# Kernel optimization log

Measured on AMD Instinct MI355X. Metric: run time of the kernel, lower is better.

Reference implementation:

```python
import jax, jax.numpy as jnp
import numpy as np

N = 65536
E = 1048576
IN_DIM = 128
POS_DIM = 128  # num_nodes (ROI one-hot dim)
HID = 128


def _mk_params(key):
    # layer 0: local in = IN_DIM + POS_DIM; layer 1: local in = HID + POS_DIM
    dims = [(IN_DIM + POS_DIM, HID), (HID + POS_DIM, HID)]
    params = {}
    for l, (din, _) in enumerate(dims):
        ks = jax.random.split(jax.random.fold_in(key, l), 4)
        params[f"l{l}_lw1"] = jax.random.normal(ks[0], (din, HID), jnp.float32) * (1.0 / np.sqrt(din))
        params[f"l{l}_lb1"] = jnp.zeros((HID,), jnp.float32)
        params[f"l{l}_lw2"] = jax.random.normal(ks[1], (HID, HID), jnp.float32) * (1.0 / np.sqrt(HID))
        params[f"l{l}_lb2"] = jnp.zeros((HID,), jnp.float32)
        params[f"l{l}_gw1"] = jax.random.normal(ks[2], (HID, HID), jnp.float32) * (1.0 / np.sqrt(HID))
        params[f"l{l}_gb1"] = jnp.zeros((HID,), jnp.float32)
        params[f"l{l}_gw2"] = jax.random.normal(ks[3], (HID, HID), jnp.float32) * (1.0 / np.sqrt(HID))
        params[f"l{l}_gb2"] = jnp.zeros((HID,), jnp.float32)
    return params


def setup_inputs() -> dict:
    key = jax.random.key(0)
    k1, k2, k3, k4 = jax.random.split(key, 4)
    inp = {
        "x": jax.random.normal(k1, (N, IN_DIM), jnp.float32),
        "pos": jax.random.normal(k2, (N, POS_DIM), jnp.float32),
        "edge_index": jax.random.randint(k3, (2, E), 0, N, jnp.int64),
    }
    inp.update(_mk_params(k4))
    return inp


def _pointnet_conv(x, pos, src, dst, lw1, lb1, lw2, lb2, gw1, gb1, gw2, gb2):
    # message: concat(x_j, pos_j - pos_i) per edge -> local_nn (Lin-ReLU-Lin)
    msg = jnp.concatenate([x[src], pos[src] - pos[dst]], axis=1)  # [E', in+pos]
    h = jax.nn.relu(msg @ lw1 + lb1) @ lw2 + lb2                  # [E', HID]
    agg = jax.ops.segment_max(h, dst, num_segments=N)             # max aggr (PointNetConv default)
    return jax.nn.relu(agg @ gw1 + gb1) @ gw2 + gb2               # global_nn


def reference(x, pos, edge_index,
              l0_lw1, l0_lb1, l0_lw2, l0_lb2, l0_gw1, l0_gb1, l0_gw2, l0_gb2,
              l1_lw1, l1_lb1, l1_lw2, l1_lb2, l1_gw1, l1_gb1, l1_gw2, l1_gb2):
    # add_self_loops=True (PointNetConv default); ensures every node has an incoming edge
    loops = jnp.arange(N, dtype=edge_index.dtype)
    src = jnp.concatenate([edge_index[0], loops])
    dst = jnp.concatenate([edge_index[1], loops])
    h = _pointnet_conv(x, pos, src, dst, l0_lw1, l0_lb1, l0_lw2, l0_lb2,
                       l0_gw1, l0_gb1, l0_gw2, l0_gb2)
    h = _pointnet_conv(h, pos, src, dst, l1_lw1, l1_lb1, l1_lw2, l1_lb2,
                       l1_gw1, l1_gb1, l1_gw2, l1_gb2)
    return h
```

## Files before the change

### kernel.cpp

```cpp
#include <hip/hip_runtime.h>
#include <hip/hip_bf16.h>
#include <stdint.h>

#define NN 65536
#define NE 1048576
#define E2 (NE + NN)
#define HID 128
#define LP 136
#define RMAX 13
#define TP 129
#define TABW 1680
#define ENC_NEG 0x007FFFFFu

typedef _Float16 h8v __attribute__((ext_vector_type(8)));
typedef __fp16 fp16x2 __attribute__((ext_vector_type(2)));
typedef __attribute__((ext_vector_type(4))) float f32x4;

__device__ __forceinline__ uint32_t pkh(float a, float b){
    union { fp16x2 h; uint32_t u; } v;
    v.h = __builtin_amdgcn_cvt_pkrtz(a, b);
    return v.u;
}
__device__ __forceinline__ uint32_t encf(float x){
    union { float f; uint32_t u; } v; v.f = x;
    return v.u ^ (uint32_t)(((int32_t)v.u >> 31) | 0x80000000);
}
__device__ __forceinline__ float decf(uint32_t u){
    union { uint32_t u; float f; } v;
    v.u = u ^ (uint32_t)(~((int32_t)u >> 31) | 0x80000000);
    return v.f;
}

__device__ __forceinline__ void gl_lds16(const _Float16* g, _Float16* l){
    __builtin_amdgcn_global_load_lds(
        (const __attribute__((address_space(1))) uint32_t*)g,
        (__attribute__((address_space(3))) uint32_t*)l, 16, 0, 0);
}

__device__ __forceinline__ void stage_copy(const _Float16* g, _Float16* l){
    const uint4* gs = (const uint4*)g; uint4* ls = (uint4*)l;
    #pragma unroll
    for (int j = 0; j < 8; j++) ls[j] = gs[j];
}
__device__ __forceinline__ void stage_cvt(const float* g, _Float16* l){
    const float4* gs = (const float4*)g; uint4* ls = (uint4*)l;
    #pragma unroll
    for (int j = 0; j < 8; j++){
        float4 f0 = gs[2*j], f1 = gs[2*j+1];
        uint4 o; o.x = pkh(f0.x, f0.y); o.y = pkh(f0.z, f0.w);
        o.z = pkh(f1.x, f1.y); o.w = pkh(f1.z, f1.w);
        ls[j] = o;
    }
}

__device__ __forceinline__ void gemm_tile(const _Float16* Ts, const _Float16* Ws,
                                          f32x4 (&acc)[2][8], int wv, int lq, int quad){
    #pragma unroll
    for (int k0 = 0; k0 < 128; k0 += 32){
        h8v af[2], bfr[8];
        #pragma unroll
        for (int rt = 0; rt < 2; rt++)
            af[rt] = *(const h8v*)(Ts + (wv*32 + rt*16 + lq)*LP + k0 + quad*8);
        #pragma unroll
        for (int ct = 0; ct < 8; ct++)
            bfr[ct] = *(const h8v*)(Ws + (ct*16 + lq)*LP + k0 + quad*8);
        #pragma unroll
        for (int rt = 0; rt < 2; rt++)
            #pragma unroll
            for (int ct = 0; ct < 8; ct++)
                acc[rt][ct] = __builtin_amdgcn_mfma_f32_16x16x32_f16(
                                  af[rt], bfr[ct], acc[rt][ct], 0, 0, 0);
    }
}

__device__ __forceinline__ void zero_acc(f32x4 (&acc)[2][8]){
    #pragma unroll
    for (int a = 0; a < 2; a++)
        #pragma unroll
        for (int b = 0; b < 8; b++)
            acc[a][b] = (f32x4){0.f, 0.f, 0.f, 0.f};
}

struct WT { const float* s[10]; _Float16* d[10]; };
__global__ void k_prep(WT w, uint32_t* cnt,
                       const float* lb2_0, const float* gw1_0, const float* gb1_0,
                       const float* lb2_1, const float* gw1_1, const float* gb1_1,
                       float* c1p){
    int b = blockIdx.x;
    if (b < 640){
        int m = b >> 6;
        int t = (b & 63) * 256 + threadIdx.x;
        int n = t >> 7, k = t & 127;
        w.d[m][n*128 + k] = (_Float16)w.s[m][k*128 + n];
    } else if (b < 896){
        cnt[(b - 640)*256 + threadIdx.x] = 1u;
    } else {
        int l = b - 896;
        int j = threadIdx.x;
        if (j < 128){
            const float* lb2 = l ? lb2_1 : lb2_0;
            const float* gw1 = l ? gw1_1 : gw1_0;
            float s = (l ? gb1_1 : gb1_0)[j];
            for (int k = 0; k < 128; k++) s += lb2[k] * gw1[k*128 + j];
            c1p[l*128 + j] = s;
        }
    }
}

__launch_bounds__(256, 2)
__global__ void k_histab3(const int* __restrict__ ei, uint32_t* __restrict__ cnt,
                          const float* __restrict__ x, const float* __restrict__ pos,
                          const _Float16* __restrict__ w1aT0, const _Float16* __restrict__ w1bT0,
                          const _Float16* __restrict__ w1bT1, const float* __restrict__ lb1_0,
                          _Float16* __restrict__ Ah, _Float16* __restrict__ Bh0,
                          _Float16* __restrict__ Bh1, uint32_t* __restrict__ agg){
    __shared__ _Float16 Ts[128*LP];
    __shared__ _Float16 Ws[128*LP];
    __shared__ float b1s[128];
    const int tid = threadIdx.x;

    if (blockIdx.x >= 512){
        int e = (blockIdx.x - 512) * 256 + tid;
        atomicAdd(&cnt[ei[NE + e]], 1u);
        return;
    }

    const int node0 = blockIdx.x * 128;
    if (tid < 128) b1s[tid] = lb1_0[tid];

    {
        uint4* ap = (uint4*)(agg + (size_t)node0 * HID);
        uint4 v = make_uint4(ENC_NEG, ENC_NEG, ENC_NEG, ENC_NEG);
        #pragma unroll
        for (int i = 0; i < 16; i++) ap[tid + i*256] = v;
    }

    const int row = tid >> 1, half = tid & 1;
    _Float16* lT = Ts + row*LP + half*64;
    _Float16* lW = Ws + row*LP + half*64;

    stage_cvt(pos + (size_t)(node0 + row)*HID + half*64, lT);
    stage_copy(w1bT0 + row*HID + half*64, lW);
    __syncthreads();

    const int wv = tid >> 6, lane = tid & 63, lq = lane & 15, quad = lane >> 4;
    f32x4 acc0[2][8], acc1[2][8];
    zero_acc(acc0);
    gemm_tile(Ts, Ws, acc0, wv, lq, quad);
    __syncthreads();

    #pragma unroll
    for (int rt = 0; rt < 2; rt++)
        #pragma unroll
        for (int ct = 0; ct < 8; ct++)
            #pragma unroll
            for (int rg = 0; rg < 4; rg++){
                int r = node0 + wv*32 + rt*16 + quad*4 + rg;
                int c = ct*16 + lq;
                Bh0[(size_t)r*HID + c] = (_Float16)acc0[rt][ct][rg];
            }
    stage_copy(w1bT1 + row*HID + half*64, lW);
    __syncthreads();

    zero_acc(acc1);
    gemm_tile(Ts, Ws, acc1, wv, lq, quad);
    __syncthreads();

    #pragma unroll
    for (int rt = 0; rt < 2; rt++)
        #pragma unroll
        for (int ct = 0; ct < 8; ct++)
            #pragma unroll
            for (int rg = 0; rg < 4; rg++){
                int r = node0 + wv*32 + rt*16 + quad*4 + rg;
                int c = ct*16 + lq;
                Bh1[(size_t)r*HID + c] = (_Float16)acc1[rt][ct][rg];
            }
    stage_cvt(x + (size_t)(node0 + row)*HID + half*64, lT);
    stage_copy(w1aT0 + row*HID + half*64, lW);
    __syncthreads();

    gemm_tile(Ts, Ws, acc0, wv, lq, quad);

    #pragma unroll
    for (int rt = 0; rt < 2; rt++)
        #pragma unroll
        for (int ct = 0; ct < 8; ct++)
            #pragma unroll
            for (int rg = 0; rg < 4; rg++){
                int r = node0 + wv*32 + rt*16 + quad*4 + rg;
                int c = ct*16 + lq;
                Ah[(size_t)r*HID + c] = (_Float16)(acc0[rt][ct][rg] + b1s[c]);
            }
}

__global__ void k_scan1(const uint32_t* __restrict__ cnt, uint32_t* __restrict__ bsum){
    __shared__ uint32_t ps[256];
    int t = threadIdx.x;
    ps[t] = cnt[blockIdx.x*256 + t]; __syncthreads();
    for (int off = 128; off > 0; off >>= 1){
        if (t < off) ps[t] += ps[t + off];
        __syncthreads();
    }
    if (t == 0) bsum[blockIdx.x] = ps[0];
}
__global__ void k_scan23(const uint32_t* __restrict__ cnt, const uint32_t* __restrict__ bsum,
                         uint32_t* __restrict__ cur){
    __shared__ uint32_t ps[256];
    __shared__ uint32_t bs[256];
    int t = threadIdx.x, b = blockIdx.x, i = b*256 + t;
    uint32_t bb = bsum[b];
    bs[t] = bsum[t];
    uint32_t v = cnt[i];
    ps[t] = v; __syncthreads();
    for (int off = 1; off < 256; off <<= 1){
        uint32_t u = (t >= off) ? ps[t - off] : 0u;
        uint32_t w = (t >= off) ? bs[t - off] : 0u;
        __syncthreads();
        ps[t] += u; bs[t] += w;
        __syncthreads();
    }
    cur[i] = (bs[b] - bb) + ps[t] - v;
}
__global__ void k_scatter(const int* __restrict__ ei, uint32_t* cur,
                          uint2* __restrict__ sedge){
    int e = blockIdx.x * 256 + threadIdx.x;
    if (e >= E2) return;
    uint32_t s, d;
    if (e < NE){ s = (uint32_t)ei[e]; d = (uint32_t)ei[NE + e]; }
    else { s = d = (uint32_t)(e - NE); }
    uint32_t p = atomicAdd(&cur[d], 1u);
    sedge[p] = make_uint2(s, d);
}

__launch_bounds__(256, 4)
__global__ void k_edge(const uint2* __restrict__ sedge,
                       const _Float16* __restrict__ Ah, const _Float16* __restrict__ Bh,
                       const _Float16* __restrict__ w2T,
                       uint32_t* __restrict__ agg){
    __shared__ _Float16 Ws[128*128];
    __shared__ __align__(16) uint32_t tab[TABW];
    __shared__ int ds_s[128];
    __shared__ unsigned long long masks_s[2];
    __shared__ int run_dst_s[RMAX];
    const int tid = threadIdx.x;
    const int bid = blockIdx.x;
    const int lb  = (bid & 7) * (E2/128/8) + (bid >> 3);
    const int e0 = lb * 128;
    const int wv = tid >> 6, lane = tid & 63, lq = lane & 15, quad = lane >> 4;
    const int r0 = wv*32 + lq, r1 = r0 + 16;

    const uint2 ea = sedge[e0 + r0];
    const uint2 eb = sedge[e0 + r1];
    int d_cur = 0;
    if (tid < 128) d_cur = (int)sedge[e0 + tid].y;

    #pragma unroll
    for (int rnd = 0; rnd < 8; rnd++){
        int g = rnd*256 + wv*64 + lane;
        int r = g >> 4, kc = g & 15;
        gl_lds16(w2T + r*HID + ((kc ^ (r & 15)) << 3),
                 Ws + rnd*2048 + wv*512);
    }

    const _Float16* a0p = Ah + (size_t)ea.x*HID + quad*8;
    const _Float16* a1p = Ah + (size_t)eb.x*HID + quad*8;
    const _Float16* b0p = Bh + (size_t)ea.y*HID + quad*8;
    const _Float16* b1p = Bh + (size_t)eb.y*HID + quad*8;
    h8v A0[4], A1[4], B0[4], B1[4];
    #pragma unroll
    for (int i = 0; i < 4; i++){
        A0[i] = *(const h8v*)(a0p + 32*i);
        A1[i] = *(const h8v*)(a1p + 32*i);
        B0[i] = *(const h8v*)(b0p + 32*i);
        B1[i] = *(const h8v*)(b1p + 32*i);
    }

    bool flag = false;
    if (tid < 128){
        ds_s[tid] = d_cur;
        int d_up  = __shfl_up(d_cur, 1);
        int d_b63 = __shfl((int)eb.y, 15);
        if (tid & 63) flag = (d_cur != d_up);
        else          flag = (tid == 0) ? true : (d_cur != d_b63);
        unsigned long long m = __ballot(flag);
        if ((tid & 63) == 0) masks_s[tid >> 6] = m;
    }
    {
        uint4* t4 = (uint4*)tab;
        const uint4 vneg = make_uint4(ENC_NEG, ENC_NEG, ENC_NEG, ENC_NEG);
        #pragma unroll
        for (int i = 0; i < 2; i++){
            int idx = tid + i*256;
            if (idx < TABW/4) t4[idx] = vneg;
        }
    }
    __syncthreads();

    const unsigned long long m0 = masks_s[0], m1 = masks_s[1];
    const int c0 = __popcll(m0);
    const int nruns = c0 + __popcll(m1);

    if (flag){
        int r;
        if (tid < 64) r = __popcll(m0 & ((2ull << tid) - 1)) - 1;
        else          r = c0 + __popcll(m1 & ((2ull << (tid-64)) - 1)) - 1;
        if (r < RMAX) run_dst_s[r] = d_cur;
    }

    f32x4 acc[2][8];
    zero_acc(acc);

    const h8v zero8 = (h8v)(_Float16)0;
    #pragma unroll
    for (int i = 0; i < 4; i++){
        h8v a0 = __builtin_elementwise_max(A0[i] - B0[i], zero8);
        h8v a1 = __builtin_elementwise_max(A1[i] - B1[i], zero8);
        const int kcb = i*4;
        #pragma unroll
        for (int ct = 0; ct < 8; ct++){
            h8v b = *(const h8v*)(Ws + (ct*16 + lq)*128 + (((kcb + quad) ^ lq) << 3));
            acc[0][ct] = __builtin_amdgcn_mfma_f32_16x16x32_f16(a0, b, acc[0][ct], 0, 0, 0);
            acc[1][ct] = __builtin_amdgcn_mfma_f32_16x16x32_f16(a1, b, acc[1][ct], 0, 0, 0);
        }
    }

    #pragma unroll
    for (int rt = 0; rt < 2; rt++){
        const int rb = wv*32 + rt*16 + quad*4;
        int rid[4];
        #pragma unroll
        for (int i = 0; i < 4; i++){
            int r = rb + i;
            if (r < 64) rid[i] = __popcll(m0 & ((2ull << r) - 1)) - 1;
            else        rid[i] = c0 + __popcll(m1 & ((2ull << (r-64)) - 1)) - 1;
        }
        const bool b01 = rid[1] != rid[0];
        const bool b12 = rid[2] != rid[1];
        const bool b23 = rid[3] != rid[2];
        #pragma unroll
        for (int ct = 0; ct < 8; ct++){
            const int c = ct*16 + lq;
            float v0 = acc[rt][ct][0], v1 = acc[rt][ct][1];
            float v2 = acc[rt][ct][2], v3 = acc[rt][ct][3];
            #define FLUSH(ID, R, V) do{ uint32_t ev = encf(V); \
                if (__builtin_expect((ID) < RMAX, 1)) atomicMax(&tab[(ID)*TP + c], ev); \
                else atomicMax(&agg[(size_t)ds_s[R]*HID + c], ev); }while(0)
            if (b01) FLUSH(rid[0], rb+0, v0); else v1 = fmaxf(v1, v0);
            if (b12) FLUSH(rid[1], rb+1, v1); else v2 = fmaxf(v2, v1);
            if (b23) FLUSH(rid[2], rb+2, v2); else v3 = fmaxf(v3, v2);
            FLUSH(rid[3], rb+3, v3);
            #undef FLUSH
        }
    }
    __syncthreads();

    {
        const int c = tid & 127;
        const int ntab = nruns < RMAX ? nruns : RMAX;
        for (int r = tid >> 7; r < ntab; r += 2){
            uint32_t v = tab[r*TP + c];
            uint32_t* dst = &agg[(size_t)run_dst_s[r]*HID + c];
            if (r == 0 || r == nruns-1 || nruns > RMAX) atomicMax(dst, v);
            else *dst = v;
        }
    }
}

__launch_bounds__(256, 2)
__global__ void k_gnn_ab(uint32_t* __restrict__ agg,
                         const _Float16* __restrict__ g1T, const _Float16* __restrict__ g2T,
                         const float* __restrict__ c1p, const float* __restrict__ gb2,
                         const _Float16* __restrict__ w1aT1, const _Float16* __restrict__ Bh1,
                         const float* __restrict__ lb1_1,
                         _Float16* __restrict__ Ah){
    __shared__ _Float16 Ts[128*LP];
    __shared__ _Float16 Ws[128*LP];
    __shared__ float c1s[128];
    __shared__ float c2s[128];
    __shared__ float b1s[128];
    const int tid = threadIdx.x;
    const int node0 = blockIdx.x * 128;
    if (tid < 128){ c1s[tid] = c1p[tid]; c2s[tid] = gb2[tid]; b1s[tid] = lb1_1[tid]; }
    const int row = tid >> 1, half = tid & 1;
    _Float16* lW = Ws + row*LP + half*64;

    {
        uint4* ga = (uint4*)(agg + (size_t)(node0 + row)*HID + half*64);
        _Float16* lt = Ts + row*LP + half*64;
        const uint4 vneg = make_uint4(ENC_NEG, ENC_NEG, ENC_NEG, ENC_NEG);
        #pragma unroll
        for (int j = 0; j < 16; j++){
            uint4 u = ga[j];
            ga[j] = vneg;
            uint2 o; o.x = pkh(decf(u.x), decf(u.y)); o.y = pkh(decf(u.z), decf(u.w));
            *(uint2*)(lt + j*4) = o;
        }
        stage_copy(g1T + row*HID + half*64, lW);
    }
    __syncthreads();

    const int wv = tid >> 6, lane = tid & 63, lq = lane & 15, quad = lane >> 4;
    f32x4 acc[2][8];
    zero_acc(acc);
    gemm_tile(Ts, Ws, acc, wv, lq, quad);
    __syncthreads();

    #pragma unroll
    for (int rt = 0; rt < 2; rt++)
        #pragma unroll
        for (int ct = 0; ct < 8; ct++)
            #pragma unroll
            for (int rg = 0; rg < 4; rg++){
                int rr = wv*32 + rt*16 + quad*4 + rg;
                int c  = ct*16 + lq;
                Ts[rr*LP + c] = (_Float16)fmaxf(acc[rt][ct][rg] + c1s[c], 0.f);
            }
    stage_copy(g2T + row*HID + half*64, lW);
    __syncthreads();

    zero_acc(acc);
    gemm_tile(Ts, Ws, acc, wv, lq, quad);
    __syncthreads();

    #pragma unroll
    for (int rt = 0; rt < 2; rt++)
        #pragma unroll
        for (int ct = 0; ct < 8; ct++)
            #pragma unroll
            for (int rg = 0; rg < 4; rg++){
                int rr = wv*32 + rt*16 + quad*4 + rg;
                int c  = ct*16 + lq;
                Ts[rr*LP + c] = (_Float16)(acc[rt][ct][rg] + c2s[c]);
            }
    stage_copy(w1aT1 + row*HID + half*64, lW);
    __syncthreads();

    zero_acc(acc);
    gemm_tile(Ts, Ws, acc, wv, lq, quad);
    __syncthreads();

    stage_copy(Bh1 + (size_t)(node0 + row)*HID + half*64, Ts + row*LP + half*64);
    __syncthreads();

    #pragma unroll
    for (int rt = 0; rt < 2; rt++)
        #pragma unroll
        for (int ct = 0; ct < 8; ct++)
            #pragma unroll
            for (int rg = 0; rg < 4; rg++){
                int rr = wv*32 + rt*16 + quad*4 + rg;
                int c  = ct*16 + lq;
                float v = acc[rt][ct][rg] + (float)Ts[rr*LP + c] + b1s[c];
                Ah[(size_t)(node0 + rr)*HID + c] = (_Float16)v;
            }
}

__launch_bounds__(256, 2)
__global__ void k_gnn(const uint32_t* __restrict__ agg,
                      const _Float16* __restrict__ g1T, const _Float16* __restrict__ g2T,
                      const float* __restrict__ c1p, const float* __restrict__ gb2,
                      float* __restrict__ outf){
    __shared__ _Float16 Ts[128*LP];
    __shared__ _Float16 Ws[128*LP];
    __shared__ float c1s[128];
    __shared__ float c2s[128];
    const int tid = threadIdx.x;
    const int node0 = blockIdx.x * 128;
    if (tid < 128){ c1s[tid] = c1p[tid]; c2s[tid] = gb2[tid]; }
    const int row = tid >> 1, half = tid & 1;
    _Float16* lW = Ws + row*LP + half*64;

    {
        const uint4* ga = (const uint4*)(agg + (size_t)(node0 + row)*HID + half*64);
        _Float16* lt = Ts + row*LP + half*64;
        #pragma unroll
        for (int j = 0; j < 16; j++){
            uint4 u = ga[j];
            uint2 o; o.x = pkh(decf(u.x), decf(u.y)); o.y = pkh(decf(u.z), decf(u.w));
            *(uint2*)(lt + j*4) = o;
        }
        stage_copy(g1T + row*HID + half*64, lW);
    }
    __syncthreads();

    const int wv = tid >> 6, lane = tid & 63, lq = lane & 15, quad = lane >> 4;
    f32x4 acc[2][8];
    zero_acc(acc);
    gemm_tile(Ts, Ws, acc, wv, lq, quad);
    __syncthreads();

    #pragma unroll
    for (int rt = 0; rt < 2; rt++)
        #pragma unroll
        for (int ct = 0; ct < 8; ct++)
            #pragma unroll
            for (int rg = 0; rg < 4; rg++){
                int rr = wv*32 + rt*16 + quad*4 + rg;
                int c  = ct*16 + lq;
                Ts[rr*LP + c] = (_Float16)fmaxf(acc[rt][ct][rg] + c1s[c], 0.f);
            }
    stage_copy(g2T + row*HID + half*64, lW);
    __syncthreads();

    zero_acc(acc);
    gemm_tile(Ts, Ws, acc, wv, lq, quad);

    #pragma unroll
    for (int rt = 0; rt < 2; rt++)
        #pragma unroll
        for (int ct = 0; ct < 8; ct++)
            #pragma unroll
            for (int rg = 0; rg < 4; rg++){
                int r = node0 + wv*32 + rt*16 + quad*4 + rg;
                int c = ct*16 + lq;
                outf[(size_t)r*HID + c] = acc[rt][ct][rg] + c2s[c];
            }
}

extern "C" void kernel_launch(void* const* d_in, const int* in_sizes, int n_in,
                              void* d_out, int out_size, void* d_ws, size_t ws_size,
                              hipStream_t stream){
    const float* x   = (const float*)d_in[0];
    const float* pos = (const float*)d_in[1];
    const int*   ei  = (const int*)d_in[2];
    const float* W[16];
    for (int i = 0; i < 16; i++) W[i] = (const float*)d_in[3 + i];

    uint8_t* p = (uint8_t*)d_ws;
    _Float16* wT[10];
    for (int i = 0; i < 10; i++) wT[i] = (_Float16*)(p + (size_t)i * 32768);
    size_t off = 10 * 32768;
    _Float16* Ah  = (_Float16*)(p + off); off += (size_t)NN * HID * 2;
    _Float16* Bh0 = (_Float16*)(p + off); off += (size_t)NN * HID * 2;
    _Float16* Bh1 = (_Float16*)(p + off); off += (size_t)NN * HID * 2;
    uint32_t* agg = (uint32_t*)(p + off); off += (size_t)NN * HID * 4;
    uint32_t* cnt = (uint32_t*)(p + off); off += (size_t)NN * 4;
    uint32_t* cur = (uint32_t*)(p + off); off += (size_t)NN * 4;
    uint32_t* bsum = (uint32_t*)(p + off); off += 256 * 4;
    uint32_t* bofs = (uint32_t*)(p + off); off += 256 * 4;
    float* c1p = (float*)(p + off); off += 256 * 4;
    uint2* sedge = (uint2*)(p + off); off += (size_t)E2 * 8;
    (void)ws_size; (void)in_sizes; (void)n_in; (void)out_size; (void)bofs;

    WT wt;
    for (int l = 0; l < 2; l++){
        wt.s[5*l + 0] = W[8*l + 0];
        wt.s[5*l + 1] = W[8*l + 0] + 128*128;
        wt.s[5*l + 2] = W[8*l + 2];
        wt.s[5*l + 3] = W[8*l + 4];
        wt.s[5*l + 4] = W[8*l + 6];
        for (int j = 0; j < 5; j++) wt.d[5*l + j] = wT[5*l + j];
    }
    k_prep<<<898, 256, 0, stream>>>(wt, cnt, W[3], W[4], W[5], W[11], W[12], W[13], c1p);

    k_histab3<<<512 + NE/256, 256, 0, stream>>>(ei, cnt, x, pos, wT[0], wT[1], wT[6],
                                                W[1], Ah, Bh0, Bh1, agg);
    k_scan1<<<256, 256, 0, stream>>>(cnt, bsum);
    k_scan23<<<256, 256, 0, stream>>>(cnt, bsum, cur);
    k_scatter<<<(E2 + 255)/256, 256, 0, stream>>>(ei, cur, sedge);

    k_edge<<<E2/128, 256, 0, stream>>>(sedge, Ah, Bh0, wT[2], agg);
    k_gnn_ab<<<NN/128, 256, 0, stream>>>(agg, wT[3], wT[4], c1p, W[7],
                                         wT[5], Bh1, W[9], Ah);
    k_edge<<<E2/128, 256, 0, stream>>>(sedge, Ah, Bh1, wT[7], agg);
    k_gnn<<<NN/128, 256, 0, stream>>>(agg, wT[8], wT[9], c1p + 128, W[15],
                                      (float*)d_out);
}
```

Before: 471.4 us.

## Shrink node GEMM tiles to 64 rows, DMA swizzled weights, overlap loads

The node-level GEMM kernels (histab3, gnn_ab, gnn) now process 64 nodes per block instead of 128. Each wave computes 16 rows, and launch bounds are raised to 3 blocks per SM, with the intent of more blocks in flight and higher occupancy. Weight tiles are loaded with the global-to-LDS DMA using an XOR swizzle shared with k_edge, and the next weight load is issued before the previous results are stored, so copying overlaps with the epilogue. The trade-off is that every weight matrix is fetched twice as many times in total, and each block gets less reuse.

```diff
diff --git a/kernel.cpp b/kernel.cpp
--- a/kernel.cpp
+++ b/kernel.cpp
@@ -37,40 +37,34 @@
         (__attribute__((address_space(3))) uint32_t*)l, 16, 0, 0);
 }
 
-__device__ __forceinline__ void stage_copy(const _Float16* g, _Float16* l){
-    const uint4* gs = (const uint4*)g; uint4* ls = (uint4*)l;
-    #pragma unroll
-    for (int j = 0; j < 8; j++) ls[j] = gs[j];
-}
-__device__ __forceinline__ void stage_cvt(const float* g, _Float16* l){
-    const float4* gs = (const float4*)g; uint4* ls = (uint4*)l;
-    #pragma unroll
-    for (int j = 0; j < 8; j++){
-        float4 f0 = gs[2*j], f1 = gs[2*j+1];
-        uint4 o; o.x = pkh(f0.x, f0.y); o.y = pkh(f0.z, f0.w);
-        o.z = pkh(f1.x, f1.y); o.w = pkh(f1.z, f1.w);
-        ls[j] = o;
-    }
-}
-
-__device__ __forceinline__ void gemm_tile(const _Float16* Ts, const _Float16* Ws,
-                                          f32x4 (&acc)[2][8], int wv, int lq, int quad){
+__device__ __forceinline__ void dma_w(const _Float16* __restrict__ wT, _Float16* Ws,
+                                      int wv, int lane){
+    #pragma unroll
+    for (int rnd = 0; rnd < 8; rnd++){
+        int g = rnd*256 + wv*64 + lane;
+        int r = g >> 4, kc = g & 15;
+        gl_lds16(wT + r*HID + ((kc ^ (r & 15)) << 3),
+                 Ws + rnd*2048 + wv*512);
+    }
+}
+
+__device__ __forceinline__ void gemm64(const _Float16* Ts, const _Float16* Ws,
+                                       f32x4 (&acc)[8], int wv, int lq, int quad){
     #pragma unroll
     for (int k0 = 0; k0 < 128; k0 += 32){
-        h8v af[2], bfr[8];
-        #pragma unroll
-        for (int rt = 0; rt < 2; rt++)
-            af[rt] = *(const h8v*)(Ts + (wv*32 + rt*16 + lq)*LP + k0 + quad*8);
-        #pragma unroll
-        for (int ct = 0; ct < 8; ct++)
-            bfr[ct] = *(const h8v*)(Ws + (ct*16 + lq)*LP + k0 + quad*8);
-        #pragma unroll
-        for (int rt = 0; rt < 2; rt++)
-            #pragma unroll
-            for (int ct = 0; ct < 8; ct++)
-                acc[rt][ct] = __builtin_amdgcn_mfma_f32_16x16x32_f16(
-                                  af[rt], bfr[ct], acc[rt][ct], 0, 0, 0);
-    }
+        h8v af = *(const h8v*)(Ts + (wv*16 + lq)*LP + k0 + quad*8);
+        const int kcb = k0 >> 3;
+        #pragma unroll
+        for (int ct = 0; ct < 8; ct++){
+            h8v b = *(const h8v*)(Ws + (ct*16 + lq)*128 + (((kcb + quad) ^ lq) << 3));
+            acc[ct] = __builtin_amdgcn_mfma_f32_16x16x32_f16(af, b, acc[ct], 0, 0, 0);
+        }
+    }
+}
+
+__device__ __forceinline__ void zero_acc8(f32x4 (&acc)[8]){
+    #pragma unroll
+    for (int b = 0; b < 8; b++) acc[b] = (f32x4){0.f, 0.f, 0.f, 0.f};
 }
 
 __device__ __forceinline__ void zero_acc(f32x4 (&acc)[2][8]){
@@ -107,91 +101,89 @@
     }
 }
 
-__launch_bounds__(256, 2)
+__launch_bounds__(256, 3)
 __global__ void k_histab3(const int* __restrict__ ei, uint32_t* __restrict__ cnt,
                           const float* __restrict__ x, const float* __restrict__ pos,
                           const _Float16* __restrict__ w1aT0, const _Float16* __restrict__ w1bT0,
                           const _Float16* __restrict__ w1bT1, const float* __restrict__ lb1_0,
                           _Float16* __restrict__ Ah, _Float16* __restrict__ Bh0,
                           _Float16* __restrict__ Bh1, uint32_t* __restrict__ agg){
-    __shared__ _Float16 Ts[128*LP];
-    __shared__ _Float16 Ws[128*LP];
+    __shared__ _Float16 Ts[64*LP];
+    __shared__ _Float16 Ws[128*128];
     __shared__ float b1s[128];
     const int tid = threadIdx.x;
 
-    if (blockIdx.x >= 512){
-        int e = (blockIdx.x - 512) * 256 + tid;
+    if (blockIdx.x >= 1024){
+        int e = (blockIdx.x - 1024) * 256 + tid;
         atomicAdd(&cnt[ei[NE + e]], 1u);
         return;
     }
 
-    const int node0 = blockIdx.x * 128;
+    const int node0 = blockIdx.x * 64;
+    const int wv = tid >> 6, lane = tid & 63, lq = lane & 15, quad = lane >> 4;
     if (tid < 128) b1s[tid] = lb1_0[tid];
 
     {
         uint4* ap = (uint4*)(agg + (size_t)node0 * HID);
         uint4 v = make_uint4(ENC_NEG, ENC_NEG, ENC_NEG, ENC_NEG);
         #pragma unroll
-        for (int i = 0; i < 16; i++) ap[tid + i*256] = v;
-    }
-
-    const int row = tid >> 1, half = tid & 1;
-    _Float16* lT = Ts + row*LP + half*64;
-    _Float16* lW = Ws + row*LP + half*64;
-
-    stage_cvt(pos + (size_t)(node0 + row)*HID + half*64, lT);
-    stage_copy(w1bT0 + row*HID + half*64, lW);
-    __syncthreads();
-
-    const int wv = tid >> 6, lane = tid & 63, lq = lane & 15, quad = lane >> 4;
-    f32x4 acc0[2][8], acc1[2][8];
-    zero_acc(acc0);
-    gemm_tile(Ts, Ws, acc0, wv, lq, quad);
-    __syncthreads();
-
-    #pragma unroll
-    for (int rt = 0; rt < 2; rt++)
-        #pragma unroll
-        for (int ct = 0; ct < 8; ct++)
-            #pragma unroll
-            for (int rg = 0; rg < 4; rg++){
-                int r = node0 + wv*32 + rt*16 + quad*4 + rg;
-                int c = ct*16 + lq;
-                Bh0[(size_t)r*HID + c] = (_Float16)acc0[rt][ct][rg];
-            }
-    stage_copy(w1bT1 + row*HID + half*64, lW);
-    __syncthreads();
-
-    zero_acc(acc1);
-    gemm_tile(Ts, Ws, acc1, wv, lq, quad);
-    __syncthreads();
-
-    #pragma unroll
-    for (int rt = 0; rt < 2; rt++)
-        #pragma unroll
-        for (int ct = 0; ct < 8; ct++)
-            #pragma unroll
-            for (int rg = 0; rg < 4; rg++){
-                int r = node0 + wv*32 + rt*16 + quad*4 + rg;
-                int c = ct*16 + lq;
-                Bh1[(size_t)r*HID + c] = (_Float16)acc1[rt][ct][rg];
-            }
-    stage_cvt(x + (size_t)(node0 + row)*HID + half*64, lT);
-    stage_copy(w1aT0 + row*HID + half*64, lW);
-    __syncthreads();
-
-    gemm_tile(Ts, Ws, acc0, wv, lq, quad);
-
-    #pragma unroll
-    for (int rt = 0; rt < 2; rt++)
-        #pragma unroll
-        for (int ct = 0; ct < 8; ct++)
-            #pragma unroll
-            for (int rg = 0; rg < 4; rg++){
-                int r = node0 + wv*32 + rt*16 + quad*4 + rg;
-                int c = ct*16 + lq;
-                Ah[(size_t)r*HID + c] = (_Float16)(acc0[rt][ct][rg] + b1s[c]);
-            }
+        for (int i = 0; i < 8; i++) ap[tid + i*256] = v;
+    }
+    #pragma unroll
+    for (int i = 0; i < 8; i++){
+        int chunk = tid + i*256;
+        int row = chunk >> 5, qc = chunk & 31;
+        float4 f = *(const float4*)(pos + (size_t)(node0 + row)*HID + qc*4);
+        uint2 o; o.x = pkh(f.x, f.y); o.y = pkh(f.z, f.w);
+        *(uint2*)(Ts + row*LP + qc*4) = o;
+    }
+    dma_w(w1bT0, Ws, wv, lane);
+    __syncthreads();
+
+    f32x4 acc0[8], acc1[8];
+    zero_acc8(acc0);
+    gemm64(Ts, Ws, acc0, wv, lq, quad);
+    __syncthreads();
+    dma_w(w1bT1, Ws, wv, lane);
+    #pragma unroll
+    for (int ct = 0; ct < 8; ct++)
+        #pragma unroll
+        for (int rg = 0; rg < 4; rg++)
+            Bh0[(size_t)(node0 + wv*16 + quad*4 + rg)*HID + ct*16 + lq]
+                = (_Float16)acc0[ct][rg];
+    __syncthreads();
+
+    zero_acc8(acc1);
+    gemm64(Ts, Ws, acc1, wv, lq, quad);
+    __syncthreads();
+
+    #pragma unroll
+    for (int i = 0; i < 8; i++){
+        int chunk = tid + i*256;
+        int row = chunk >> 5, qc = chunk & 31;
+        float4 f = *(const float4*)(x + (size_t)(node0 + row)*HID + qc*4);
+        uint2 o; o.x = pkh(f.x, f.y); o.y = pkh(f.z, f.w);
+        *(uint2*)(Ts + row*LP + qc*4) = o;
+    }
+    dma_w(w1aT0, Ws, wv, lane);
+    #pragma unroll
+    for (int ct = 0; ct < 8; ct++)
+        #pragma unroll
+        for (int rg = 0; rg < 4; rg++)
+            Bh1[(size_t)(node0 + wv*16 + quad*4 + rg)*HID + ct*16 + lq]
+                = (_Float16)acc1[ct][rg];
+    __syncthreads();
+
+    gemm64(Ts, Ws, acc0, wv, lq, quad);
+
+    #pragma unroll
+    for (int ct = 0; ct < 8; ct++)
+        #pragma unroll
+        for (int rg = 0; rg < 4; rg++){
+            int c = ct*16 + lq;
+            Ah[(size_t)(node0 + wv*16 + quad*4 + rg)*HID + c]
+                = (_Float16)(acc0[ct][rg] + b1s[c]);
+        }
 }
 
 __global__ void k_scan1(const uint32_t* __restrict__ cnt, uint32_t* __restrict__ bsum){
@@ -255,13 +247,7 @@
     int d_cur = 0;
     if (tid < 128) d_cur = (int)sedge[e0 + tid].y;
 
-    #pragma unroll
-    for (int rnd = 0; rnd < 8; rnd++){
-        int g = rnd*256 + wv*64 + lane;
-        int r = g >> 4, kc = g & 15;
-        gl_lds16(w2T + r*HID + ((kc ^ (r & 15)) << 3),
-                 Ws + rnd*2048 + wv*512);
-    }
+    dma_w(w2T, Ws, wv, lane);
 
     const _Float16* a0p = Ah + (size_t)ea.x*HID + quad*8;
     const _Float16* a1p = Ah + (size_t)eb.x*HID + quad*8;
@@ -367,155 +353,137 @@
     }
 }
 
-__launch_bounds__(256, 2)
+__launch_bounds__(256, 3)
 __global__ void k_gnn_ab(uint32_t* __restrict__ agg,
                          const _Float16* __restrict__ g1T, const _Float16* __restrict__ g2T,
                          const float* __restrict__ c1p, const float* __restrict__ gb2,
                          const _Float16* __restrict__ w1aT1, const _Float16* __restrict__ Bh1,
                          const float* __restrict__ lb1_1,
                          _Float16* __restrict__ Ah){
-    __shared__ _Float16 Ts[128*LP];
-    __shared__ _Float16 Ws[128*LP];
+    __shared__ _Float16 Ts[64*LP];
+    __shared__ _Float16 Ws[128*128];
     __shared__ float c1s[128];
     __shared__ float c2s[128];
     __shared__ float b1s[128];
     const int tid = threadIdx.x;
-    const int node0 = blockIdx.x * 128;
+    const int node0 = blockIdx.x * 64;
+    const int wv = tid >> 6, lane = tid & 63, lq = lane & 15, quad = lane >> 4;
     if (tid < 128){ c1s[tid] = c1p[tid]; c2s[tid] = gb2[tid]; b1s[tid] = lb1_1[tid]; }
-    const int row = tid >> 1, half = tid & 1;
-    _Float16* lW = Ws + row*LP + half*64;
 
     {
-        uint4* ga = (uint4*)(agg + (size_t)(node0 + row)*HID + half*64);
-        _Float16* lt = Ts + row*LP + half*64;
         const uint4 vneg = make_uint4(ENC_NEG, ENC_NEG, ENC_NEG, ENC_NEG);
         #pragma unroll
-        for (int j = 0; j < 16; j++){
-            uint4 u = ga[j];
-            ga[j] = vneg;
+        for (int i = 0; i < 8; i++){
+            int chunk = tid + i*256;
+            int row = chunk >> 5, qc = chunk & 31;
+            uint4* ga = (uint4*)(agg + (size_t)(node0 + row)*HID + qc*4);
+            uint4 u = *ga; *ga = vneg;
             uint2 o; o.x = pkh(decf(u.x), decf(u.y)); o.y = pkh(decf(u.z), decf(u.w));
-            *(uint2*)(lt + j*4) = o;
-        }
-        stage_copy(g1T + row*HID + half*64, lW);
-    }
-    __syncthreads();
-
-    const int wv = tid >> 6, lane = tid & 63, lq = lane & 15, quad = lane >> 4;
-    f32x4 acc[2][8];
-    zero_acc(acc);
-    gemm_tile(Ts, Ws, acc, wv, lq, quad);
-    __syncthreads();
-
-    #pragma unroll
-    for (int rt = 0; rt < 2; rt++)
-        #pragma unroll
-        for (int ct = 0; ct < 8; ct++)
-            #pragma unroll
-            for (int rg = 0; rg < 4; rg++){
-                int rr = wv*32 + rt*16 + quad*4 + rg;
-                int c  = ct*16 + lq;
-                Ts[rr*LP + c] = (_Float16)fmaxf(acc[rt][ct][rg] + c1s[c], 0.f);
-            }
-    stage_copy(g2T + row*HID + half*64, lW);
-    __syncthreads();
-
-    zero_acc(acc);
-    gemm_tile(Ts, Ws, acc, wv, lq, quad);
-    __syncthreads();
-
-    #pragma unroll
-    for (int rt = 0; rt < 2; rt++)
-        #pragma unroll
-        for (int ct = 0; ct < 8; ct++)
-            #pragma unroll
-            for (int rg = 0; rg < 4; rg++){
-                int rr = wv*32 + rt*16 + quad*4 + rg;
-                int c  = ct*16 + lq;
-                Ts[rr*LP + c] = (_Float16)(acc[rt][ct][rg] + c2s[c]);
-            }
-    stage_copy(w1aT1 + row*HID + half*64, lW);
-    __syncthreads();
-
-    zero_acc(acc);
-    gemm_tile(Ts, Ws, acc, wv, lq, quad);
-    __syncthreads();
-
-    stage_copy(Bh1 + (size_t)(node0 + row)*HID + half*64, Ts + row*LP + half*64);
-    __syncthreads();
-
-    #pragma unroll
-    for (int rt = 0; rt < 2; rt++)
-        #pragma unroll
-        for (int ct = 0; ct < 8; ct++)
-            #pragma unroll
-            for (int rg = 0; rg < 4; rg++){
-                int rr = wv*32 + rt*16 + quad*4 + rg;
-                int c  = ct*16 + lq;
-                float v = acc[rt][ct][rg] + (float)Ts[rr*LP + c] + b1s[c];
-                Ah[(size_t)(node0 + rr)*HID + c] = (_Float16)v;
-            }
-}
-
-__launch_bounds__(256, 2)
+            *(uint2*)(Ts + row*LP + qc*4) = o;
+        }
+    }
+    dma_w(g1T, Ws, wv, lane);
+    __syncthreads();
+
+    f32x4 acc[8];
+    zero_acc8(acc);
+    gemm64(Ts, Ws, acc, wv, lq, quad);
+    __syncthreads();
+    dma_w(g2T, Ws, wv, lane);
+    #pragma unroll
+    for (int ct = 0; ct < 8; ct++)
+        #pragma unroll
+        for (int rg = 0; rg < 4; rg++){
+            int c = ct*16 + lq;
+            Ts[(wv*16 + quad*4 + rg)*LP + c] = (_Float16)fmaxf(acc[ct][rg] + c1s[c], 0.f);
+        }
+    __syncthreads();
+
+    zero_acc8(acc);
+    gemm64(Ts, Ws, acc, wv, lq, quad);
+    __syncthreads();
+    dma_w(w1aT1, Ws, wv, lane);
+    #pragma unroll
+    for (int ct = 0; ct < 8; ct++)
+        #pragma unroll
+        for (int rg = 0; rg < 4; rg++){
+            int c = ct*16 + lq;
+            Ts[(wv*16 + quad*4 + rg)*LP + c] = (_Float16)(acc[ct][rg] + c2s[c]);
+        }
+    __syncthreads();
+
+    _Float16 bres[8][4];
+    #pragma unroll
+    for (int ct = 0; ct < 8; ct++)
+        #pragma unroll
+        for (int rg = 0; rg < 4; rg++)
+            bres[ct][rg] = Bh1[(size_t)(node0 + wv*16 + quad*4 + rg)*HID + ct*16 + lq];
+
+    zero_acc8(acc);
+    gemm64(Ts, Ws, acc, wv, lq, quad);
+
+    #pragma unroll
+    for (int ct = 0; ct < 8; ct++)
+        #pragma unroll
+        for (int rg = 0; rg < 4; rg++){
+            int c = ct*16 + lq;
+            float v = acc[ct][rg] + (float)bres[ct][rg] + b1s[c];
+            Ah[(size_t)(node0 + wv*16 + quad*4 + rg)*HID + c] = (_Float16)v;
+        }
+}
+
+__launch_bounds__(256, 3)
 __global__ void k_gnn(const uint32_t* __restrict__ agg,
                       const _Float16* __restrict__ g1T, const _Float16* __restrict__ g2T,
                       const float* __restrict__ c1p, const float* __restrict__ gb2,
                       float* __restrict__ outf){
-    __shared__ _Float16 Ts[128*LP];
-    __shared__ _Float16 Ws[128*LP];
+    __shared__ _Float16 Ts[64*LP];
+    __shared__ _Float16 Ws[128*128];
     __shared__ float c1s[128];
     __shared__ float c2s[128];
     const int tid = threadIdx.x;
-    const int node0 = blockIdx.x * 128;
+    const int node0 = blockIdx.x * 64;
+    const int wv = tid >> 6, lane = tid & 63, lq = lane & 15, quad = lane >> 4;
     if (tid < 128){ c1s[tid] = c1p[tid]; c2s[tid] = gb2[tid]; }
-    const int row = tid >> 1, half = tid & 1;
-    _Float16* lW = Ws + row*LP + half*64;
 
     {
-        const uint4* ga = (const uint4*)(agg + (size_t)(node0 + row)*HID + half*64);
-        _Float16* lt = Ts + row*LP + half*64;
-        #pragma unroll
-        for (int j = 0; j < 16; j++){
-            uint4 u = ga[j];
+        #pragma unroll
+        for (int i = 0; i < 8; i++){
+            int chunk = tid + i*256;
+            int row = chunk >> 5, qc = chunk & 31;
+            const uint4* ga = (const uint4*)(agg + (size_t)(node0 + row)*HID + qc*4);
+            uint4 u = *ga;
             uint2 o; o.x = pkh(decf(u.x), decf(u.y)); o.y = pkh(decf(u.z), decf(u.w));
-            *(uint2*)(lt + j*4) = o;
-        }
-        stage_copy(g1T + row*HID + half*64, lW);
-    }
-    __syncthreads();
-
-    const int wv = tid >> 6, lane = tid & 63, lq = lane & 15, quad = lane >> 4;
-    f32x4 acc[2][8];
-    zero_acc(acc);
-    gemm_tile(Ts, Ws, acc, wv, lq, quad);
-    __syncthreads();
-
-    #pragma unroll
-    for (int rt = 0; rt < 2; rt++)
-        #pragma unroll
-        for (int ct = 0; ct < 8; ct++)
-            #pragma unroll
-            for (int rg = 0; rg < 4; rg++){
-                int rr = wv*32 + rt*16 + quad*4 + rg;
-                int c  = ct*16 + lq;
-                Ts[rr*LP + c] = (_Float16)fmaxf(acc[rt][ct][rg] + c1s[c], 0.f);
-            }
-    stage_copy(g2T + row*HID + half*64, lW);
-    __syncthreads();
-
-    zero_acc(acc);
-    gemm_tile(Ts, Ws, acc, wv, lq, quad);
-
-    #pragma unroll
-    for (int rt = 0; rt < 2; rt++)
-        #pragma unroll
-        for (int ct = 0; ct < 8; ct++)
-            #pragma unroll
-            for (int rg = 0; rg < 4; rg++){
-                int r = node0 + wv*32 + rt*16 + quad*4 + rg;
-                int c = ct*16 + lq;
-                outf[(size_t)r*HID + c] = acc[rt][ct][rg] + c2s[c];
-            }
+            *(uint2*)(Ts + row*LP + qc*4) = o;
+        }
+    }
+    dma_w(g1T, Ws, wv, lane);
+    __syncthreads();
+
+    f32x4 acc[8];
+    zero_acc8(acc);
+    gemm64(Ts, Ws, acc, wv, lq, quad);
+    __syncthreads();
+    dma_w(g2T, Ws, wv, lane);
+    #pragma unroll
+    for (int ct = 0; ct < 8; ct++)
+        #pragma unroll
+        for (int rg = 0; rg < 4; rg++){
+            int c = ct*16 + lq;
+            Ts[(wv*16 + quad*4 + rg)*LP + c] = (_Float16)fmaxf(acc[ct][rg] + c1s[c], 0.f);
+        }
+    __syncthreads();
+
+    zero_acc8(acc);
+    gemm64(Ts, Ws, acc, wv, lq, quad);
+
+    #pragma unroll
+    for (int ct = 0; ct < 8; ct++)
+        #pragma unroll
+        for (int rg = 0; rg < 4; rg++){
+            int c = ct*16 + lq;
+            outf[(size_t)(node0 + wv*16 + quad*4 + rg)*HID + c] = acc[ct][rg] + c2s[c];
+        }
 }
 
 extern "C" void kernel_launch(void* const* d_in, const int* in_sizes, int n_in,
@@ -554,16 +522,16 @@
     }
     k_prep<<<898, 256, 0, stream>>>(wt, cnt, W[3], W[4], W[5], W[11], W[12], W[13], c1p);
 
-    k_histab3<<<512 + NE/256, 256, 0, stream>>>(ei, cnt, x, pos, wT[0], wT[1], wT[6],
-                                                W[1], Ah, Bh0, Bh1, agg);
+    k_histab3<<<1024 + NE/256, 256, 0, stream>>>(ei, cnt, x, pos, wT[0], wT[1], wT[6],
+                                                 W[1], Ah, Bh0, Bh1, agg);
     k_scan1<<<256, 256, 0, stream>>>(cnt, bsum);
     k_scan23<<<256, 256, 0, stream>>>(cnt, bsum, cur);
     k_scatter<<<(E2 + 255)/256, 256, 0, stream>>>(ei, cur, sedge);
 
     k_edge<<<E2/128, 256, 0, stream>>>(sedge, Ah, Bh0, wT[2], agg);
-    k_gnn_ab<<<NN/128, 256, 0, stream>>>(agg, wT[3], wT[4], c1p, W[7],
-                                         wT[5], Bh1, W[9], Ah);
+    k_gnn_ab<<<NN/64, 256, 0, stream>>>(agg, wT[3], wT[4], c1p, W[7],
+                                        wT[5], Bh1, W[9], Ah);
     k_edge<<<E2/128, 256, 0, stream>>>(sedge, Ah, Bh1, wT[7], agg);
-    k_gnn<<<NN/128, 256, 0, stream>>>(agg, wT[8], wT[9], c1p + 128, W[15],
-                                      (float*)d_out);
-}
+    k_gnn<<<NN/64, 256, 0, stream>>>(agg, wT[8], wT[9], c1p + 128, W[15],
+                                     (float*)d_out);
+}
```

Result: faster. 452.4 us (-4.0%).
